# Kernel optimization log

Measured on AMD Instinct MI355X. Metric: run time of the kernel, lower is better.

Reference implementation:

```python
import jax, jax.numpy as jnp
import numpy as np
from math import factorial, sqrt

L_MAX = 3
L_MAX_OUT = 3
NUM_SHELLS = 3
NUM_SH = (L_MAX + 1) ** 2  # 16 spherical-harmonic kernel components
SPLIT = [2 * l + 1 for l in range(L_MAX + 1)]  # [1,3,5,7]


def _su2_cg(j1, m1, j2, m2, j3, m3):
    """Clebsch-Gordan coefficient <j1 m1 j2 m2 | j3 m3> via the Racah formula."""
    if m3 != m1 + m2:
        return 0.0
    f = factorial
    vmin = max(-j1 + j2 + m3, -j1 + m1, 0)
    vmax = min(j2 + j3 + m1, j3 - j1 + j2, j3 + m3)
    c = sqrt((2 * j3 + 1) * f(j3 + j1 - j2) * f(j3 - j1 + j2) * f(j1 + j2 - j3) / f(j1 + j2 + j3 + 1)
             * f(j3 + m3) * f(j3 - m3) / (f(j1 - m1) * f(j1 + m1) * f(j2 - m2) * f(j2 + m2)))
    s = 0.0
    for v in range(vmin, vmax + 1):
        s += (-1.0) ** (v + j2 + m2) * f(j2 + j3 + m1 - v) * f(j1 - m1 + v) / (
            f(v) * f(j3 - j1 + j2 - v) * f(j3 + m3 - v) * f(v + j1 - j2 - m3))
    return c * s


def _real_to_complex(l):
    q = np.zeros((2 * l + 1, 2 * l + 1), dtype=np.complex128)
    for m in range(-l, 0):
        q[l + m, l + abs(m)] = 1 / sqrt(2)
        q[l + m, l - abs(m)] = -1j / sqrt(2)
    q[l, l] = 1.0
    for m in range(1, l + 1):
        q[l + m, l + abs(m)] = (-1) ** m / sqrt(2)
        q[l + m, l - abs(m)] = 1j * (-1) ** m / sqrt(2)
    return (-1j) ** l * q  # phase makes the real-basis CG purely real


def _real_cg(j, l, J):
    # CG coupling tensor in the real spherical-harmonic basis, shape (2j+1, 2l+1, 2J+1)
    C = np.zeros((2 * j + 1, 2 * l + 1, 2 * J + 1))
    for m1 in range(-j, j + 1):
        for m2 in range(-l, l + 1):
            for m3 in range(-J, J + 1):
                C[j + m1, l + m2, J + m3] = _su2_cg(j, m1, l, m2, J, m3)
    Cr = np.einsum('ij,kl,mn,ikm->jln', _real_to_complex(j), _real_to_complex(l),
                   np.conj(_real_to_complex(J)), C.astype(np.complex128))
    return np.real(Cr).astype(np.float32)  # imaginary part vanishes by phase choice


_CG = {(j, l, J): jnp.asarray(_real_cg(j, l, J))
       for j in range(1, L_MAX + 1) for l in range(1, L_MAX + 1)
       for J in range(abs(j - l), min(j + l, L_MAX_OUT) + 1)}


def setup_inputs() -> dict:
    key = jax.random.key(0)
    ks = jax.random.split(key, 6)
    b, n_src, n_tgt, p, C = 2, 4096, 2048, 32, 32
    return {
        'f0': jax.random.normal(ks[0], (b, n_src, 1, C), jnp.float32),
        'f1': jax.random.normal(ks[1], (b, n_src, 3, C), jnp.float32),
        'f2': jax.random.normal(ks[2], (b, n_src, 5, C), jnp.float32),
        'f3': jax.random.normal(ks[3], (b, n_src, 7, C), jnp.float32),
        'kernels': jax.random.normal(ks[4], (b, n_tgt, p, NUM_SH, NUM_SHELLS), jnp.float32),
        'patches_idx': jax.random.randint(ks[5], (b, n_tgt, p), 0, n_src, jnp.int32),
    }


def reference(f0, f1, f2, f3, kernels, patches_idx):
    feats = [f0, f1, f2, f3]
    b, n_src = f0.shape[0], f0.shape[1]
    ch_split = [(2 * l + 1) * feats[l].shape[-1] for l in range(L_MAX + 1)]
    # flatten each degree block and concatenate: (b, n_src, sum (2l+1)*C_l)
    signal = jnp.concatenate([f.reshape(b, n_src, -1) for f in feats], axis=-1)
    # gather per-target-point patches: (b, n_tgt, p, Ct)
    patches = jax.vmap(lambda s, i: s[i])(signal, patches_idx)
    n_tgt, p = patches_idx.shape[1], patches_idx.shape[2]
    S = kernels.shape[-1]
    K = kernels.reshape(b, n_tgt, p, -1)  # (b, n_tgt, p, NUM_SH*S)
    # kernel-weighted patch contraction
    y = jnp.einsum('bvpy,bvpc->bvyc', K, patches)  # (b, n_tgt, NUM_SH*S, Ct)
    y_parts = jnp.split(y, list(np.cumsum(ch_split)[:-1]), axis=-1)
    sh_cuts = list(np.cumsum(SPLIT)[:-1])
    out = {J: [] for J in range(L_MAX_OUT + 1)}
    cg_terms = []
    for l in range(L_MAX + 1):
        Cl = feats[l].shape[-1]
        yi = y_parts[l].reshape(b, n_tgt, NUM_SH, S, 2 * l + 1, Cl)
        yi = jnp.transpose(yi, (0, 1, 2, 4, 3, 5)).reshape(b, n_tgt, NUM_SH, 2 * l + 1, S * Cl)
        yjs = jnp.split(yi, sh_cuts, axis=2)
        for j in range(L_MAX + 1):
            yij = yjs[j]  # (b, n_tgt, 2j+1, 2l+1, S*Cl)
            if l == 0:
                out[j].append(yij[:, :, :, 0, :])
            elif j == 0:
                out[l].append(yij[:, :, 0, :, :])
            else:
                cg_terms.append((j, l, yij))
    # sparse Clebsch-Gordan tensor-product decomposition
    for j, l, yij in cg_terms:
        for J in range(abs(j - l), min(j + l, L_MAX_OUT) + 1):
            out[J].append(jnp.einsum('xyz,bvxyc->bvzc', _CG[(j, l, J)], yij))
    return tuple(jnp.concatenate(out[J], axis=-1) for J in range(L_MAX_OUT + 1))
```

## Files before the change

### kernel.cpp

```cpp
#include <hip/hip_runtime.h>
#include <hip/hip_bf16.h>

#define NTGT 2048
#define NSRC 4096
#define NPATCH 32
#define NY 48
#define PITCH 136
#define NCG2 3524
#define NSLOTS 1280
#define DESC_OFF 16384

using short8 = __attribute__((ext_vector_type(8))) short;
using f32x4  = __attribute__((ext_vector_type(4))) float;

#define NTERMS 34
__constant__ int T_j[NTERMS]    = {0,1,2,3, 1,0,1,2,1,2,3,2,3, 2,0,1,2,3,1,2,3,1,2,3, 3,0,2,3,1,2,3,1,2,3};
__constant__ int T_l[NTERMS]    = {0,1,2,3, 0,1,1,1,2,2,2,3,3, 0,2,1,1,1,2,2,2,3,3,3, 0,3,1,1,2,2,2,3,3,3};
__constant__ int T_Jv[NTERMS]   = {0,0,0,0, 1,1,1,1,1,1,1,1,1, 2,2,2,2,2,2,2,2,2,2,2, 3,3,3,3,3,3,3,3,3,3};
__constant__ int T_col[NTERMS]  = {0,1,2,3, 0,1,2,3,4,5,6,7,8, 0,1,2,3,4,5,6,7,8,9,10, 0,1,2,3,4,5,6,7,8,9};
__constant__ int OUT_BASE[4] = {0, 1572864, 12189696, 33816576};
__constant__ int OUT_W[4]    = {384, 864, 1056, 960};
__constant__ int NJW_C[4]    = {384, 2592, 5280, 6720};
__constant__ int LI_L[16]  = {0,1,1,1,2,2,2,2,2,3,3,3,3,3,3,3};
__constant__ int LI_ML[16] = {0,0,1,2,0,1,2,3,4,0,1,2,3,4,5,6};
__constant__ int LI_WQ[16] = {1,3,3,3,5,5,5,5,5,7,7,7,7,7,7,7};
__constant__ int TERM_SLOT[NTERMS] = {1088,1024,384,0, 1094,1184,1030,896,768,390,256,128,6,
                                      1112,1202,1048,914,640,786,408,274,512,146,24,
                                      1142,1232,944,670,816,438,304,542,176,54};
__constant__ int CG2OFF4[NTERMS] = {0,0,3,10, 0,0,23,32,44,56,77,104,131,
                                    0,0,170,185,205,235,255,290,335,365,410,
                                    0,0,475,503,545,573,622,685,727,790};
__constant__ int RND_CLASS[20] = {0,0,1,1,2,2,3,3,4,4,5,5,6,6,7,7,8,9,9,9};
__constant__ signed char WAVE_RNDS[8][3] = {
  {0,17,-1},{1,16,-1},{2,8,-1},{3,9,18},{4,10,19},{5,11,-1},{6,14,13},{7,15,12}};

__device__ double factd(int n) { double r = 1.0; for (int i = 2; i <= n; ++i) r *= i; return r; }

__device__ double su2_cg(int j1, int m1, int j2, int m2, int j3, int m3) {
  if (m3 != m1 + m2) return 0.0;
  int vmin = max(max(-j1 + j2 + m3, -j1 + m1), 0);
  int vmax = min(min(j2 + j3 + m1, j3 - j1 + j2), j3 + m3);
  double cc = sqrt((2.0*j3 + 1.0) * factd(j3 + j1 - j2) * factd(j3 - j1 + j2) * factd(j1 + j2 - j3)
                   / factd(j1 + j2 + j3 + 1)
                   * factd(j3 + m3) * factd(j3 - m3)
                   / (factd(j1 - m1) * factd(j1 + m1) * factd(j2 - m2) * factd(j2 + m2)));
  double s = 0.0;
  for (int v = vmin; v <= vmax; ++v) {
    double sgn = ((v + j2 + m2) & 1) ? -1.0 : 1.0;
    s += sgn * factd(j2 + j3 + m1 - v) * factd(j1 - m1 + v)
         / (factd(v) * factd(j3 - j1 + j2 - v) * factd(j3 + m3 - v) * factd(v + j1 - j2 - m3));
  }
  return cc * s;
}

struct C2 { double re, im; };

__device__ C2 qent(int l, int r, int c) {
  double re = 0.0, im = 0.0;
  const double is2 = 0.70710678118654752440;
  int m = r - l;
  if (m < 0) {
    if (c == l - m) re = is2;
    else if (c == l + m) im = -is2;
  } else if (m == 0) {
    if (c == l) re = 1.0;
  } else {
    double sgn = (m & 1) ? -1.0 : 1.0;
    if (c == l + m) re = sgn * is2;
    else if (c == l - m) im = sgn * is2;
  }
  const double pr[4] = {1.0, 0.0, -1.0, 0.0};
  const double pi[4] = {0.0, -1.0, 0.0, 1.0};
  double a = pr[l & 3], bb = pi[l & 3];
  C2 o; o.re = re * a - im * bb; o.im = re * bb + im * a; return o;
}

__global__ void cg_init_kernel(float* __restrict__ cg2) {
  __shared__ double su2_tab[49];
  const int t = blockIdx.x;
  const int j = T_j[t], l = T_l[t], J = T_Jv[t];
  if (j == 0 || l == 0) return;
  const int nj = 2*j + 1, nl = 2*l + 1, nJ = 2*J + 1;
  const int njnl = nj * nl, stride4 = (njnl + 3) >> 2;
  for (int ik = threadIdx.x; ik < njnl; ik += blockDim.x) {
    int i = ik / nl, k = ik - (ik / nl) * nl;
    int m = (i - j) + (k - l) + J;
    su2_tab[ik] = (m >= 0 && m <= 2*J) ? su2_cg(j, i - j, l, k - l, J, m - J) : 0.0;
  }
  __syncthreads();
  const int n = nJ * njnl;
  for (int e = threadIdx.x; e < n; e += blockDim.x) {
    const int z = e / njnl, rr = e - (e / njnl) * njnl;
    const int mj = rr / nl, ml = rr - (rr / nl) * nl;
    double acc = 0.0;
    for (int i = 0; i < nj; ++i) {
      for (int k = 0; k < nl; ++k) {
        int m = (i - j) + (k - l) + J;
        if (m < 0 || m > 2*J) continue;
        double s2 = su2_tab[i * nl + k];
        if (s2 == 0.0) continue;
        C2 qa = qent(j, i, mj), qb = qent(l, k, ml), qc = qent(J, m, z);
        double r1 = qa.re * qb.re - qa.im * qb.im;
        double i1 = qa.re * qb.im + qa.im * qb.re;
        acc += (r1 * qc.re + i1 * qc.im) * s2;
      }
    }
    cg2[(CG2OFF4[t] + z * stride4) * 4 + rr] = (float)acc;
  }
}

__global__ void desc_init_kernel(uint2* __restrict__ desc) {
  const int t = blockIdx.x;
  const int j = T_j[t], l = T_l[t], J = T_Jv[t];
  const int n = (2*J + 1) * 6;
  const int slot0 = TERM_SLOT[t];
  const bool cp = (j == 0 || l == 0);
  const int nl = 2*l + 1, njnl = (2*j + 1) * nl;
  const int stride4 = (njnl + 3) >> 2;
  for (int i = threadIdx.x; i < n; i += blockDim.x) {
    const int z = i / 6, r = i - (i / 6) * 6;
    const int s = r >> 1, ch4 = r & 1;
    const unsigned ob = (unsigned)(OUT_BASE[J] + T_col[t] * 96 + s * 32 + ch4 * 4 + z * OUT_W[J]);
    int ybase;
    if (!cp)         ybase = (j*j*3 + s) * PITCH + l*l*8 + ch4*4;
    else if (l == 0) ybase = ((j*j + z)*3 + s) * PITCH + ch4*4;
    else             ybase = s * PITCH + (l*l + z)*8 + ch4*4;
    const unsigned cgb4 = (unsigned)(CG2OFF4[t] + z * stride4);
    desc[slot0 + i] = make_uint2(ob,
        (unsigned)(ybase >> 2) | (cgb4 << 11) | ((unsigned)J << 21) | 0x80000000u);
  }
}

__device__ __forceinline__ unsigned bfb(float x) {
  union { __hip_bfloat16 h; unsigned short u; } c;
  c.h = __float2bfloat16(x);
  return (unsigned)c.u;
}

template<int JT, int LT>
__device__ __forceinline__ float4 pairc(const float4* __restrict__ yb4,
                                        const float* __restrict__ cgp) {
  constexpr int nl = 2*LT + 1, njnl = (2*JT + 1) * nl;
  float a0 = 0.f, a1 = 0.f, a2 = 0.f, a3 = 0.f;
  #pragma unroll
  for (int e = 0; e < njnl; ++e) {
    const int mj = e / nl, ml = e - (e / nl) * nl;
    const float4 yq = yb4[mj * 102 + ml * 2];
    const float c = cgp[e];
    a0 = fmaf(c, yq.x, a0); a1 = fmaf(c, yq.y, a1);
    a2 = fmaf(c, yq.z, a2); a3 = fmaf(c, yq.w, a3);
  }
  float4 o; o.x = a0; o.y = a1; o.z = a2; o.w = a3; return o;
}

__global__ __launch_bounds__(512, 6) void sh_conv_kernel(
    const float* __restrict__ f0, const float* __restrict__ f1,
    const float* __restrict__ f2, const float* __restrict__ f3,
    const float* __restrict__ kern, const int* __restrict__ pidx,
    const float* __restrict__ cg2, const uint2* __restrict__ desc,
    float* __restrict__ out) {
  __shared__ float y_lds[NY * PITCH];
  __shared__ float cg_lds[NCG2];
  const int tid = threadIdx.x;
  const int lane = tid & 63, wid = tid >> 6;
  const int g = lane >> 4, lr = lane & 15;
  const int xcd  = blockIdx.x & 7;
  const int slot = blockIdx.x >> 3;
  const int bv   = ((slot >> 2) << 3) | xcd;
  const int cb   = slot & 3;
  const int b    = bv >> 11;

  const int* ip = pidx + (size_t)bv * NPATCH;
  int idx8[8];
  #pragma unroll
  for (int r = 0; r < 8; ++r) idx8[r] = ip[g * 8 + r];

  const float* kB = kern + (size_t)bv * (NPATCH * NY);
  float afv[3][8];
  #pragma unroll
  for (int m = 0; m < 3; ++m)
    #pragma unroll
    for (int r = 0; r < 8; ++r)
      afv[m][r] = kB[(g*8 + r) * NY + m*16 + lr];

  const int li  = wid * 2 + (lr >> 3);
  const int chl = lr & 7;
  const int l_  = LI_L[li], mlv = LI_ML[li], wq = LI_WQ[li];
  const float* fp = (l_ == 0) ? f0 : (l_ == 1) ? f1 : (l_ == 2) ? f2 : f3;
  const float* base = fp + ((size_t)b * NSRC) * (wq * 32) + mlv * 32 + cb * 8 + chl;
  float bv8[8];
  #pragma unroll
  for (int r = 0; r < 8; ++r) bv8[r] = base[(size_t)(idx8[r] * wq) << 5];

  for (int i = tid; i < NCG2; i += 512) cg_lds[i] = cg2[i];

  short8 afr[3];
  #pragma unroll
  for (int m = 0; m < 3; ++m) {
    short8 af;
    #pragma unroll
    for (int r = 0; r < 8; ++r) af[r] = (short)bfb(afv[m][r]);
    afr[m] = af;
  }
  short8 bfr;
  #pragma unroll
  for (int r = 0; r < 8; ++r) bfr[r] = (short)bfb(bv8[r]);

  f32x4 acc0 = {0.f,0.f,0.f,0.f}, acc1 = {0.f,0.f,0.f,0.f}, acc2 = {0.f,0.f,0.f,0.f};
  acc0 = __builtin_amdgcn_mfma_f32_16x16x32_bf16(afr[0], bfr, acc0, 0, 0, 0);
  acc1 = __builtin_amdgcn_mfma_f32_16x16x32_bf16(afr[1], bfr, acc1, 0, 0, 0);
  acc2 = __builtin_amdgcn_mfma_f32_16x16x32_bf16(afr[2], bfr, acc2, 0, 0, 0);

  #pragma unroll
  for (int q = 0; q < 4; ++q) {
    y_lds[(0*16 + g*4 + q) * PITCH + wid*16 + lr] = acc0[q];
    y_lds[(1*16 + g*4 + q) * PITCH + wid*16 + lr] = acc1[q];
    y_lds[(2*16 + g*4 + q) * PITCH + wid*16 + lr] = acc2[q];
  }

  __syncthreads();

  const int widu = __builtin_amdgcn_readfirstlane(wid);
  const float4* yall = (const float4*)y_lds;
  #pragma unroll 1
  for (int ri = 0; ri < 3; ++ri) {
    const int rnd = WAVE_RNDS[widu][ri];
    if (rnd < 0) break;
    const uint2 d = desc[(rnd << 6) | lane];
    const unsigned w1 = d.y;
    const float4* yb4 = yall + (w1 & 0x7FF);
    const float*  cgp = cg_lds + (((w1 >> 11) & 0x3FF) << 2);
    const int J = (w1 >> 21) & 3;
    float4 o;
    switch (RND_CLASS[rnd]) {
      case 0: o = pairc<3,3>(yb4, cgp); break;
      case 1: o = pairc<2,3>(yb4, cgp); break;
      case 2: o = pairc<3,2>(yb4, cgp); break;
      case 3: o = pairc<2,2>(yb4, cgp); break;
      case 4: o = pairc<1,3>(yb4, cgp); break;
      case 5: o = pairc<3,1>(yb4, cgp); break;
      case 6: o = pairc<1,2>(yb4, cgp); break;
      case 7: o = pairc<2,1>(yb4, cgp); break;
      case 8: o = pairc<1,1>(yb4, cgp); break;
      default: o = yb4[0]; break;
    }
    if (w1 >> 31)
      *(float4*)&out[(size_t)d.x + (size_t)bv * NJW_C[J] + cb * 8] = o;
  }
}

extern "C" void kernel_launch(void* const* d_in, const int* in_sizes, int n_in,
                              void* d_out, int out_size, void* d_ws, size_t ws_size,
                              hipStream_t stream) {
  const float* f0   = (const float*)d_in[0];
  const float* f1   = (const float*)d_in[1];
  const float* f2   = (const float*)d_in[2];
  const float* f3   = (const float*)d_in[3];
  const float* kern = (const float*)d_in[4];
  const int*   pidx = (const int*)d_in[5];
  float* out  = (float*)d_out;
  float* cg2  = (float*)d_ws;
  uint2* desc = (uint2*)((char*)d_ws + DESC_OFF);

  hipMemsetAsync(desc, 0, NSLOTS * sizeof(uint2), stream);
  hipLaunchKernelGGL(cg_init_kernel, dim3(NTERMS), dim3(256), 0, stream, cg2);
  hipLaunchKernelGGL(desc_init_kernel, dim3(NTERMS), dim3(64), 0, stream, desc);
  hipLaunchKernelGGL(sh_conv_kernel, dim3(4 * 2 * NTGT), dim3(512), 0, stream,
                     f0, f1, f2, f3, kern, pidx, cg2, desc, out);
}
```

Before: 210.3 us.

## Process two channel blocks per workgroup, reusing kernel fragments and CG table

Each workgroup now handles two adjacent 8-channel blocks for the same target point instead of one, which halves the grid size. The kernel weights, patch indices and CG table load into LDS are done once and reused for both blocks. Both feature gathers are issued up front, and the two MFMA/CG phases run in sequence with an extra barrier between them. Launch bounds also move from 6 to 8 waves per EU, which tightens register limits and may cause spilling. The per-block work becomes more serial.

New measurement: 266.3 us. 1.27x slower.

```diff
diff --git a/kernel.cpp b/kernel.cpp
--- a/kernel.cpp
+++ b/kernel.cpp
@@ -153,74 +153,11 @@
   float4 o; o.x = a0; o.y = a1; o.z = a2; o.w = a3; return o;
 }
 
-__global__ __launch_bounds__(512, 6) void sh_conv_kernel(
-    const float* __restrict__ f0, const float* __restrict__ f1,
-    const float* __restrict__ f2, const float* __restrict__ f3,
-    const float* __restrict__ kern, const int* __restrict__ pidx,
-    const float* __restrict__ cg2, const uint2* __restrict__ desc,
-    float* __restrict__ out) {
-  __shared__ float y_lds[NY * PITCH];
-  __shared__ float cg_lds[NCG2];
-  const int tid = threadIdx.x;
-  const int lane = tid & 63, wid = tid >> 6;
-  const int g = lane >> 4, lr = lane & 15;
-  const int xcd  = blockIdx.x & 7;
-  const int slot = blockIdx.x >> 3;
-  const int bv   = ((slot >> 2) << 3) | xcd;
-  const int cb   = slot & 3;
-  const int b    = bv >> 11;
-
-  const int* ip = pidx + (size_t)bv * NPATCH;
-  int idx8[8];
-  #pragma unroll
-  for (int r = 0; r < 8; ++r) idx8[r] = ip[g * 8 + r];
-
-  const float* kB = kern + (size_t)bv * (NPATCH * NY);
-  float afv[3][8];
-  #pragma unroll
-  for (int m = 0; m < 3; ++m)
-    #pragma unroll
-    for (int r = 0; r < 8; ++r)
-      afv[m][r] = kB[(g*8 + r) * NY + m*16 + lr];
-
-  const int li  = wid * 2 + (lr >> 3);
-  const int chl = lr & 7;
-  const int l_  = LI_L[li], mlv = LI_ML[li], wq = LI_WQ[li];
-  const float* fp = (l_ == 0) ? f0 : (l_ == 1) ? f1 : (l_ == 2) ? f2 : f3;
-  const float* base = fp + ((size_t)b * NSRC) * (wq * 32) + mlv * 32 + cb * 8 + chl;
-  float bv8[8];
-  #pragma unroll
-  for (int r = 0; r < 8; ++r) bv8[r] = base[(size_t)(idx8[r] * wq) << 5];
-
-  for (int i = tid; i < NCG2; i += 512) cg_lds[i] = cg2[i];
-
-  short8 afr[3];
-  #pragma unroll
-  for (int m = 0; m < 3; ++m) {
-    short8 af;
-    #pragma unroll
-    for (int r = 0; r < 8; ++r) af[r] = (short)bfb(afv[m][r]);
-    afr[m] = af;
-  }
-  short8 bfr;
-  #pragma unroll
-  for (int r = 0; r < 8; ++r) bfr[r] = (short)bfb(bv8[r]);
-
-  f32x4 acc0 = {0.f,0.f,0.f,0.f}, acc1 = {0.f,0.f,0.f,0.f}, acc2 = {0.f,0.f,0.f,0.f};
-  acc0 = __builtin_amdgcn_mfma_f32_16x16x32_bf16(afr[0], bfr, acc0, 0, 0, 0);
-  acc1 = __builtin_amdgcn_mfma_f32_16x16x32_bf16(afr[1], bfr, acc1, 0, 0, 0);
-  acc2 = __builtin_amdgcn_mfma_f32_16x16x32_bf16(afr[2], bfr, acc2, 0, 0, 0);
-
-  #pragma unroll
-  for (int q = 0; q < 4; ++q) {
-    y_lds[(0*16 + g*4 + q) * PITCH + wid*16 + lr] = acc0[q];
-    y_lds[(1*16 + g*4 + q) * PITCH + wid*16 + lr] = acc1[q];
-    y_lds[(2*16 + g*4 + q) * PITCH + wid*16 + lr] = acc2[q];
-  }
-
-  __syncthreads();
-
-  const int widu = __builtin_amdgcn_readfirstlane(wid);
+__device__ __forceinline__ void phase2(const float* __restrict__ y_lds,
+                                       const float* __restrict__ cg_lds,
+                                       const uint2* __restrict__ desc,
+                                       float* __restrict__ out,
+                                       int widu, int lane, int bv, int cb) {
   const float4* yall = (const float4*)y_lds;
   #pragma unroll 1
   for (int ri = 0; ri < 3; ++ri) {
@@ -249,6 +186,105 @@
   }
 }
 
+__global__ __launch_bounds__(512, 8) void sh_conv_kernel(
+    const float* __restrict__ f0, const float* __restrict__ f1,
+    const float* __restrict__ f2, const float* __restrict__ f3,
+    const float* __restrict__ kern, const int* __restrict__ pidx,
+    const float* __restrict__ cg2, const uint2* __restrict__ desc,
+    float* __restrict__ out) {
+  __shared__ float y_lds[NY * PITCH];
+  __shared__ float cg_lds[NCG2];
+  const int tid = threadIdx.x;
+  const int lane = tid & 63, wid = tid >> 6;
+  const int g = lane >> 4, lr = lane & 15;
+  const int xcd  = blockIdx.x & 7;
+  const int s2   = blockIdx.x >> 3;
+  const int cbA  = (s2 & 1) * 2;
+  const int cbB  = cbA + 1;
+  const int bv   = ((s2 >> 1) << 3) | xcd;
+  const int b    = bv >> 11;
+
+  const int* ip = pidx + (size_t)bv * NPATCH;
+  int idx8[8];
+  #pragma unroll
+  for (int r = 0; r < 8; ++r) idx8[r] = ip[g * 8 + r];
+
+  const float* kB = kern + (size_t)bv * (NPATCH * NY);
+  float afv[3][8];
+  #pragma unroll
+  for (int m = 0; m < 3; ++m)
+    #pragma unroll
+    for (int r = 0; r < 8; ++r)
+      afv[m][r] = kB[(g*8 + r) * NY + m*16 + lr];
+
+  const int li  = wid * 2 + (lr >> 3);
+  const int chl = lr & 7;
+  const int l_  = LI_L[li], mlv = LI_ML[li], wq = LI_WQ[li];
+  const float* fp = (l_ == 0) ? f0 : (l_ == 1) ? f1 : (l_ == 2) ? f2 : f3;
+  const float* baseA = fp + ((size_t)b * NSRC) * (wq * 32) + mlv * 32 + cbA * 8 + chl;
+  float bvA[8], bvB[8];
+  #pragma unroll
+  for (int r = 0; r < 8; ++r) {
+    const size_t ro = (size_t)(idx8[r] * wq) << 5;
+    bvA[r] = baseA[ro];
+    bvB[r] = baseA[ro + 8];
+  }
+
+  for (int i = tid; i < NCG2; i += 512) cg_lds[i] = cg2[i];
+
+  short8 afr[3];
+  #pragma unroll
+  for (int m = 0; m < 3; ++m) {
+    short8 af;
+    #pragma unroll
+    for (int r = 0; r < 8; ++r) af[r] = (short)bfb(afv[m][r]);
+    afr[m] = af;
+  }
+
+  short8 bfrA;
+  #pragma unroll
+  for (int r = 0; r < 8; ++r) bfrA[r] = (short)bfb(bvA[r]);
+  {
+    f32x4 a0 = {0.f,0.f,0.f,0.f}, a1 = {0.f,0.f,0.f,0.f}, a2 = {0.f,0.f,0.f,0.f};
+    a0 = __builtin_amdgcn_mfma_f32_16x16x32_bf16(afr[0], bfrA, a0, 0, 0, 0);
+    a1 = __builtin_amdgcn_mfma_f32_16x16x32_bf16(afr[1], bfrA, a1, 0, 0, 0);
+    a2 = __builtin_amdgcn_mfma_f32_16x16x32_bf16(afr[2], bfrA, a2, 0, 0, 0);
+    #pragma unroll
+    for (int q = 0; q < 4; ++q) {
+      y_lds[(0*16 + g*4 + q) * PITCH + wid*16 + lr] = a0[q];
+      y_lds[(1*16 + g*4 + q) * PITCH + wid*16 + lr] = a1[q];
+      y_lds[(2*16 + g*4 + q) * PITCH + wid*16 + lr] = a2[q];
+    }
+  }
+  short8 bfrB;
+  #pragma unroll
+  for (int r = 0; r < 8; ++r) bfrB[r] = (short)bfb(bvB[r]);
+
+  __syncthreads();
+
+  const int widu = __builtin_amdgcn_readfirstlane(wid);
+  phase2(y_lds, cg_lds, desc, out, widu, lane, bv, cbA);
+
+  __syncthreads();
+
+  {
+    f32x4 a0 = {0.f,0.f,0.f,0.f}, a1 = {0.f,0.f,0.f,0.f}, a2 = {0.f,0.f,0.f,0.f};
+    a0 = __builtin_amdgcn_mfma_f32_16x16x32_bf16(afr[0], bfrB, a0, 0, 0, 0);
+    a1 = __builtin_amdgcn_mfma_f32_16x16x32_bf16(afr[1], bfrB, a1, 0, 0, 0);
+    a2 = __builtin_amdgcn_mfma_f32_16x16x32_bf16(afr[2], bfrB, a2, 0, 0, 0);
+    #pragma unroll
+    for (int q = 0; q < 4; ++q) {
+      y_lds[(0*16 + g*4 + q) * PITCH + wid*16 + lr] = a0[q];
+      y_lds[(1*16 + g*4 + q) * PITCH + wid*16 + lr] = a1[q];
+      y_lds[(2*16 + g*4 + q) * PITCH + wid*16 + lr] = a2[q];
+    }
+  }
+
+  __syncthreads();
+
+  phase2(y_lds, cg_lds, desc, out, widu, lane, bv, cbB);
+}
+
 extern "C" void kernel_launch(void* const* d_in, const int* in_sizes, int n_in,
                               void* d_out, int out_size, void* d_ws, size_t ws_size,
                               hipStream_t stream) {
@@ -265,6 +301,6 @@
   hipMemsetAsync(desc, 0, NSLOTS * sizeof(uint2), stream);
   hipLaunchKernelGGL(cg_init_kernel, dim3(NTERMS), dim3(256), 0, stream, cg2);
   hipLaunchKernelGGL(desc_init_kernel, dim3(NTERMS), dim3(64), 0, stream, desc);
-  hipLaunchKernelGGL(sh_conv_kernel, dim3(4 * 2 * NTGT), dim3(512), 0, stream,
+  hipLaunchKernelGGL(sh_conv_kernel, dim3(2 * 2 * NTGT), dim3(512), 0, stream,
                      f0, f1, f2, f3, kern, pidx, cg2, desc, out);
 }
```
